# Kernel optimization log

Hardware: AMD Instinct MI355X
Metric: run time of the kernel (lower is better)

The kernel has to match this reference:

```python
import jax, jax.numpy as jnp
import numpy as np

B, CI, HW, K, C, NH, L = 512, 3, 28, 28 // 28 and 0 or 7, 1024, 16, 12
K = 7


def setup_inputs() -> dict:
    key = jax.random.key(0)
    ks = jax.random.split(key, 8)
    s = 0.02
    return {
        "x": jax.random.normal(ks[0], (B, CI, HW, HW), jnp.float32),
        "conv_w": jax.random.normal(ks[1], (C, CI, K, K), jnp.float32) * s,  # Conv2d weight [Co,Ci,k,k], shared with deconv
        "ln1_w": jnp.ones((L, C), jnp.float32),
        "ln1_b": jnp.zeros((L, C), jnp.float32),
        "wq": jax.random.normal(ks[2], (L, C, C), jnp.float32) * s,
        "wk": jax.random.normal(ks[3], (L, C, C), jnp.float32) * s,
        "wv": jax.random.normal(ks[4], (L, C, C), jnp.float32) * s,
        "ln2_w": jnp.ones((L, C), jnp.float32),
        "ln2_b": jnp.zeros((L, C), jnp.float32),
        "mlp_w": jax.random.normal(ks[5], (L, C, C), jnp.float32) * s,
        "mlp_b": jnp.zeros((L, C), jnp.float32),
        "out_w": jax.random.normal(ks[6], (C, C), jnp.float32) * s,
        "out_b": jnp.zeros((C,), jnp.float32),
        "head_num": NH,
    }


def _layernorm(x, w, b, eps=1e-5):
    m = jnp.mean(x, axis=-1, keepdims=True)
    v = jnp.var(x, axis=-1, keepdims=True)  # biased var, matches torch LayerNorm
    return (x - m) * jax.lax.rsqrt(v + eps) * w + b


def _attn(h, wq, wk, wv, nh):
    b, t, c = h.shape
    hd = c // nh
    q = (h @ wq.T).reshape(b, t, nh, hd).transpose(0, 2, 1, 3)  # [B,H,T,hd]
    k = (h @ wk.T).reshape(b, t, nh, hd).transpose(0, 2, 1, 3)
    v = (h @ wv.T).reshape(b, t, nh, hd).transpose(0, 2, 1, 3)
    scores = jnp.einsum("bhqd,bhkd->bhqk", q, k) / jnp.sqrt(jnp.float32(hd))
    mask = jnp.tril(jnp.ones((t, t), bool))
    scores = jnp.where(mask, scores, -jnp.inf)
    a = jax.nn.softmax(scores, axis=-1)
    o = jnp.einsum("bhqk,bhkd->bhqd", a, v)
    return o.transpose(0, 2, 1, 3).reshape(b, t, c)


def _forward(x, conv_w, ln1_w, ln1_b, wq, wk, wv, ln2_w, ln2_b, mlp_w, mlp_b, out_w, out_b, head_num):
    b, ci, hh, ww = x.shape
    co, _, k, _ = conv_w.shape
    # thumbnail: bilinear downsample to (k,k) (align_corners=False == half-pixel), then k-strided conv -> [B,Co]
    thumb = jax.image.resize(x, (b, ci, k, k), method="bilinear", antialias=False)
    thumb_tok = jnp.einsum("bcpq,dcpq->bd", thumb, conv_w)
    # kernel==stride conv == patchify + matmul
    hp, wp = hh // k, ww // k
    xp = x.reshape(b, ci, hp, k, wp, k)
    patches = jnp.einsum("bcipjq,dcpq->bdij", xp, conv_w).reshape(b, co, hp * wp)
    h = jnp.concatenate([thumb_tok[:, :, None], patches], axis=-1).transpose(0, 2, 1)  # [B,T=1+hp*wp,C]
    nlayers = ln1_w.shape[0]
    for l in range(nlayers):
        a = _attn(_layernorm(h, ln1_w[l], ln1_b[l]), wq[l], wk[l], wv[l], head_num)
        h = h + a
        m = _layernorm(h, ln2_w[l], ln2_b[l]) @ mlp_w[l].T + mlp_b[l]
        h = h + m
    logits = h @ out_w.T + out_b  # [B,T,C]
    # decode: ConvTranspose2d(kernel=stride=k) with shared weight; input [B,Co,1,T] -> [B,Ci,k,T*k]
    z = logits.transpose(0, 2, 1)  # [B,Co,T]
    t = z.shape[-1]
    out = jnp.einsum("bcs,cdhw->bdhsw", z, conv_w).reshape(b, ci, k, t * k)
    return out


def reference(x, conv_w, ln1_w, ln1_b, wq, wk, wv, ln2_w, ln2_b, mlp_w, mlp_b, out_w, out_b, head_num):
    return _forward(x, conv_w, ln1_w, ln1_b, wq, wk, wv, ln2_w, ln2_b, mlp_w, mlp_b, out_w, out_b, head_num)
```

## Files before the change

### kernel.cpp

```cpp
#include <hip/hip_runtime.h>


typedef unsigned short u16;
typedef short bfrag8 __attribute__((ext_vector_type(8)));
typedef float facc4 __attribute__((ext_vector_type(4)));

__device__ __forceinline__ u16 f2bf(float f) {
  union { float f; unsigned u; } x; x.f = f;
  unsigned r = x.u + 0x7fffu + ((x.u >> 16) & 1u);
  return (u16)(r >> 16);
}
__device__ __forceinline__ float bf2f(u16 h) {
  union { unsigned u; float f; } x; x.u = ((unsigned)h) << 16;
  return x.f;
}


template <int QM>
__device__ __forceinline__ void loadA(const u16* S, int sb, int aBase, int swz,
                                      bfrag8 (&aF)[4][2])
{
  const int base = sb + QM * 8192 + aBase;
#pragma unroll
  for (int im = 0; im < 4; ++im) {
    aF[im][0] = *(const bfrag8*)&S[base + im * 1024 + swz];
    aF[im][1] = *(const bfrag8*)&S[base + im * 1024 + (swz ^ 32)];
  }
}

template <int QN>
__device__ __forceinline__ void loadB(const u16* S, int sb, int bBase, int swz,
                                      bfrag8 (&bF)[2][2])
{
  const int base = sb + 16384 + QN * 8192 + bBase;
#pragma unroll
  for (int in = 0; in < 2; ++in) {
    bF[in][0] = *(const bfrag8*)&S[base + in * 1024 + swz];
    bF[in][1] = *(const bfrag8*)&S[base + in * 1024 + (swz ^ 32)];
  }
}

template <int QM, int QN>
__device__ __forceinline__ void pmfma(bfrag8 (&aF)[4][2], bfrag8 (&bF)[2][2],
                                      facc4 (&acc)[8][4])
{
#pragma unroll
  for (int im = 0; im < 4; ++im)
#pragma unroll
    for (int in = 0; in < 2; ++in) {
      facc4 c = acc[QM * 4 + im][QN * 2 + in];
      c = __builtin_amdgcn_mfma_f32_16x16x32_bf16(aF[im][0], bF[in][0], c, 0, 0, 0);
      c = __builtin_amdgcn_mfma_f32_16x16x32_bf16(aF[im][1], bF[in][1], c, 0, 0, 0);
      acc[QM * 4 + im][QN * 2 + in] = c;
    }
}

template <int MODE>
__global__ __launch_bounds__(512, 2) void gemm256(
    const u16* __restrict__ A, int lda,
    const u16* __restrict__ B0, const u16* __restrict__ B1, const u16* __restrict__ B2,
    int ldb, int K, int cpx,
    void* __restrict__ outp, long long zstride, int ldo,
    const float* __restrict__ bias)
{
  __shared__ u16 S[65536];

  const int bid = blockIdx.x;
  const int wg = (bid & 7) * cpx + (bid >> 3);
  const int perz = 34 * 4;
  const int z = wg / perz;
  const int r0 = wg - z * perz;
  const int y = r0 >> 2;
  const int x = r0 & 3;
  const int m0 = y * 256, n0 = x * 256;
  const u16* __restrict__ B = (z == 0) ? B0 : ((z == 1) ? B1 : B2);

  const int tid = threadIdx.x;
  const int wave = tid >> 6;
  const int lane = tid & 63;
  const int lrow = lane & 15, lquad = lane >> 4;
  const int mh = wave >> 2;
  const int w4 = wave & 3;
  const int wm = mh * 128, wn = w4 * 64;

  const int swz = (lquad ^ (lrow & 7)) * 8;
  const int aBase = mh * 4096 + lrow * 64;
  const int bBase = w4 * 2048 + lrow * 64;

  const int l3 = lane >> 3;
  const int kc = ((lane & 7) ^ l3) * 8;
  const int arow0 = mh * 128 + (wave & 3) * 16 + l3;
  const int arow1 = arow0 + 8;
  const int w20 = wave * 2, w21 = wave * 2 + 1;
  const int brow0 = (w20 >> 2) * 64 + (w20 & 3) * 8 + l3;
  const int brow1 = (w21 >> 2) * 64 + (w21 & 3) * 8 + l3;
  const u16* gA0 = A + (long long)(m0 + arow0) * lda + kc;
  const u16* gA1 = A + (long long)(m0 + arow1) * lda + kc;
  const u16* gB0 = B + (long long)(n0 + brow0) * ldb + kc;
  const u16* gB1 = B + (long long)(n0 + brow1) * ldb + kc;
  const long long aq = 64LL * lda;
  const long long bq = 32LL * ldb;
  const int ldsW = wave * 1024 + lane * 8;

  auto stageA = [&](int qm, int tt) {
    u16* d0 = S + ((tt & 1) * 32768 + qm * 8192) + ldsW;
    __builtin_amdgcn_global_load_lds((const __attribute__((address_space(1))) void*)(gA0 + qm * aq + tt * 64),
                                     (__attribute__((address_space(3))) void*)d0, 16, 0, 0);
    __builtin_amdgcn_global_load_lds((const __attribute__((address_space(1))) void*)(gA1 + qm * aq + tt * 64),
                                     (__attribute__((address_space(3))) void*)(d0 + 512), 16, 0, 0);
  };
  auto stageB = [&](int qn, int tt) {
    u16* d0 = S + ((tt & 1) * 32768 + 16384 + qn * 8192) + ldsW;
    __builtin_amdgcn_global_load_lds((const __attribute__((address_space(1))) void*)(gB0 + qn * bq + tt * 64),
                                     (__attribute__((address_space(3))) void*)d0, 16, 0, 0);
    __builtin_amdgcn_global_load_lds((const __attribute__((address_space(1))) void*)(gB1 + qn * bq + tt * 64),
                                     (__attribute__((address_space(3))) void*)(d0 + 512), 16, 0, 0);
  };

  facc4 acc[8][4] = {};

  stageA(0, 0); stageB(0, 0); stageA(1, 0); stageB(1, 0); stageA(0, 1);
  asm volatile("s_waitcnt vmcnt(6)" ::: "memory");
  __builtin_amdgcn_sched_barrier(0);
  __builtin_amdgcn_s_barrier();

  const int NT = K >> 6;
  bfrag8 aF[4][2], bF[2][2];
  for (int t = 0; t < NT; ++t) {
    const int sb = (t & 1) * 32768;
    {
      loadA<0>(S, sb, aBase, swz, aF);
      loadB<0>(S, sb, bBase, swz, bF);
      if (t + 1 < NT) stageB(0, t + 1);
      __builtin_amdgcn_sched_barrier(0);
      __builtin_amdgcn_s_barrier();
      asm volatile("s_waitcnt lgkmcnt(0)" ::: "memory");
      __builtin_amdgcn_sched_barrier(0);
      __builtin_amdgcn_s_setprio(1);
      pmfma<0, 0>(aF, bF, acc);
      __builtin_amdgcn_s_setprio(0);
      if (t + 1 < NT) asm volatile("s_waitcnt vmcnt(4)" ::: "memory");
      else            asm volatile("s_waitcnt vmcnt(0)" ::: "memory");
      __builtin_amdgcn_sched_barrier(0);
      __builtin_amdgcn_s_barrier();
    }
    {
      loadB<1>(S, sb, bBase, swz, bF);
      if (t + 1 < NT) stageA(1, t + 1);
      __builtin_amdgcn_sched_barrier(0);
      __builtin_amdgcn_s_barrier();
      asm volatile("s_waitcnt lgkmcnt(0)" ::: "memory");
      __builtin_amdgcn_sched_barrier(0);
      __builtin_amdgcn_s_setprio(1);
      pmfma<0, 1>(aF, bF, acc);
      __builtin_amdgcn_s_setprio(0);
      __builtin_amdgcn_sched_barrier(0);
      __builtin_amdgcn_s_barrier();
    }
    {
      loadA<1>(S, sb, aBase, swz, aF);
      if (t + 1 < NT) stageB(1, t + 1);
      __builtin_amdgcn_sched_barrier(0);
      __builtin_amdgcn_s_barrier();
      asm volatile("s_waitcnt lgkmcnt(0)" ::: "memory");
      __builtin_amdgcn_sched_barrier(0);
      __builtin_amdgcn_s_setprio(1);
      pmfma<1, 1>(aF, bF, acc);
      __builtin_amdgcn_s_setprio(0);
      if (t + 2 < NT) asm volatile("s_waitcnt vmcnt(4)" ::: "memory");
      else            asm volatile("s_waitcnt vmcnt(0)" ::: "memory");
      __builtin_amdgcn_sched_barrier(0);
      __builtin_amdgcn_s_barrier();
    }
    {
      loadB<0>(S, sb, bBase, swz, bF);
      if (t + 2 < NT) stageA(0, t + 2);
      __builtin_amdgcn_sched_barrier(0);
      __builtin_amdgcn_s_barrier();
      asm volatile("s_waitcnt lgkmcnt(0)" ::: "memory");
      __builtin_amdgcn_sched_barrier(0);
      __builtin_amdgcn_s_setprio(1);
      pmfma<1, 0>(aF, bF, acc);
      __builtin_amdgcn_s_setprio(0);
      __builtin_amdgcn_sched_barrier(0);
      __builtin_amdgcn_s_barrier();
    }
  }

#pragma unroll
  for (int in = 0; in < 4; ++in) {
    const int col = n0 + wn + in * 16 + lrow;
    const float bb = bias ? bias[col] : 0.0f;
#pragma unroll
    for (int im = 0; im < 8; ++im) {
#pragma unroll
      for (int r = 0; r < 4; ++r) {
        const int row = m0 + wm + im * 16 + lquad * 4 + r;
        const float v = acc[im][in][r] + bb;
        if (MODE == 1) {
          (((u16*)outp) + zstride * z)[(long long)row * ldo + col] = f2bf(v);
        } else if (MODE == 2) {
          ((float*)outp)[(long long)row * ldo + col] += v;
        } else {
          const long long off = (long long)row * ldo + col;
          const float nv = ((float*)outp)[off] + v;
          ((float*)outp)[off] = nv;
          ((u16*)zstride)[off] = f2bf(nv);
        }
      }
    }
  }
}

template <int MODE>
__global__ __launch_bounds__(256) void gemm_bt(
    const u16* __restrict__ A, int lda,
    const u16* __restrict__ B0, const u16* __restrict__ B1, const u16* __restrict__ B2,
    int ldb, int K, int NX,
    void* __restrict__ outp, long long zstride, int ldo,
    const float* __restrict__ bias)
{
  __shared__ __align__(16) u16 As[8192];
  __shared__ __align__(16) u16 Bs[8192];

  const int l = blockIdx.x;
  const int xcd = l & 7;
  const int j = l >> 3;
  const int per_epoch = 9 * NX;
  const int z = j / per_epoch;
  const int r2 = j - z * per_epoch;
  const int g = r2 / NX;
  const int y = xcd + 8 * g;
  if (y >= 68) return;
  const int x = r2 - g * NX;
  const int n0 = x * 128;
  const int m0 = y * 128;
  const u16* __restrict__ B = (z == 0) ? B0 : ((z == 1) ? B1 : B2);

  const int tid  = threadIdx.x;
  const int wave = tid >> 6;
  const int lane = tid & 63;
  const int wm   = (wave >> 1) * 64;
  const int wn   = (wave & 1) * 64;
  const int lrow = lane & 15;
  const int lquad = lane >> 4;

  facc4 acc[4][4] = {};

  const u16* ga[4]; const u16* gb[4];
#pragma unroll
  for (int j2 = 0; j2 < 4; ++j2) {
    const int s = tid + 256 * j2;
    const int t = s >> 9, s2 = s & 511;
    const int r = s2 >> 2, c = (s2 & 3) + 4 * t;
    ga[j2] = A + (long long)(m0 + r) * lda + c * 8;
    gb[j2] = B + (long long)(n0 + r) * ldb + c * 8;
  }

  const int aoff = (wm + lrow) * 32 + lquad * 8;
  const int boff = (wn + lrow) * 32 + lquad * 8;

  for (int k0 = 0; k0 < K; k0 += 64) {
#pragma unroll
    for (int j2 = 0; j2 < 4; ++j2) {
      __builtin_amdgcn_global_load_lds((const __attribute__((address_space(1))) void*)ga[j2],
                                       (__attribute__((address_space(3))) void*)(As + (tid + 256 * j2) * 8), 16, 0, 0);
      __builtin_amdgcn_global_load_lds((const __attribute__((address_space(1))) void*)gb[j2],
                                       (__attribute__((address_space(3))) void*)(Bs + (tid + 256 * j2) * 8), 16, 0, 0);
      ga[j2] += 64; gb[j2] += 64;
    }
    __syncthreads();

#pragma unroll
    for (int t = 0; t < 2; ++t) {
      bfrag8 af[4], bfr[4];
#pragma unroll
      for (int im = 0; im < 4; ++im) af[im] = *(const bfrag8*)(As + t * 4096 + aoff + 512 * im);
#pragma unroll
      for (int in = 0; in < 4; ++in) bfr[in] = *(const bfrag8*)(Bs + t * 4096 + boff + 512 * in);
#pragma unroll
      for (int im = 0; im < 4; ++im)
#pragma unroll
        for (int in = 0; in < 4; ++in)
          acc[im][in] = __builtin_amdgcn_mfma_f32_16x16x32_bf16(af[im], bfr[in], acc[im][in], 0, 0, 0);
    }
    __syncthreads();
  }

#pragma unroll
  for (int in = 0; in < 4; ++in) {
    const int col = n0 + wn + in * 16 + lrow;
    const float bb = bias ? bias[col] : 0.0f;
#pragma unroll
    for (int im = 0; im < 4; ++im) {
#pragma unroll
      for (int r = 0; r < 4; ++r) {
        const int row = m0 + wm + im * 16 + lquad * 4 + r;
        const float v = acc[im][in][r] + bb;
        if (MODE == 0) {
          ((float*)outp)[(long long)row * ldo + col] = v;
        } else if (MODE == 1) {
          (((u16*)outp) + zstride * z)[(long long)row * ldo + col] = f2bf(v);
        } else if (MODE == 2) {
          ((float*)outp)[(long long)row * ldo + col] += v;
        } else if (MODE == 4) {
          const long long off = (long long)row * ldo + col;
          const float nv = ((float*)outp)[off] + v;
          ((float*)outp)[off] = nv;
          ((u16*)zstride)[off] = f2bf(nv);
        } else {
          if (col < 147) {
            const int b = row / 17, s = row - b * 17;
            const int d = col / 49, rem = col - d * 49;
            const int hk = rem / 7, wk = rem - hk * 7;
            ((float*)outp)[(long long)((b * 3 + d) * 7 + hk) * 119 + s * 7 + wk] = v;
          }
        }
      }
    }
  }
}

__global__ __launch_bounds__(256) void ln_kernel(
    const float* __restrict__ h, const float* __restrict__ w,
    const float* __restrict__ b, u16* __restrict__ out)
{
  const long long row = blockIdx.x;
  const int t = threadIdx.x;
  const float4 v = ((const float4*)(h + row * 1024))[t];
  float s = v.x + v.y + v.z + v.w;
  float q = v.x * v.x + v.y * v.y + v.z * v.z + v.w * v.w;
  for (int o = 32; o > 0; o >>= 1) { s += __shfl_down(s, o); q += __shfl_down(q, o); }
  __shared__ float ss[4], sq[4];
  const int wave = t >> 6, lane = t & 63;
  if (lane == 0) { ss[wave] = s; sq[wave] = q; }
  __syncthreads();
  const float st = ss[0] + ss[1] + ss[2] + ss[3];
  const float qt = sq[0] + sq[1] + sq[2] + sq[3];
  const float mean = st * (1.0f / 1024.0f);
  const float var = qt * (1.0f / 1024.0f) - mean * mean;
  const float inv = rsqrtf(var + 1e-5f);
  const float4 w4 = ((const float4*)w)[t];
  const float4 b4 = ((const float4*)b)[t];
  ushort4 o;
  o.x = f2bf((v.x - mean) * inv * w4.x + b4.x);
  o.y = f2bf((v.y - mean) * inv * w4.y + b4.y);
  o.z = f2bf((v.z - mean) * inv * w4.z + b4.z);
  o.w = f2bf((v.w - mean) * inv * w4.w + b4.w);
  ((ushort4*)(out + row * 1024))[t] = o;
}

__global__ __launch_bounds__(256) void attn_kernel(const u16* __restrict__ QKV,
                                                   float* __restrict__ h)
{
  const int blk = blockIdx.x;
  const int b = blk >> 4, head = blk & 15;
  __shared__ float qs[17][64], ks[17][64], vs[17][64];
  __shared__ float sc[17][20];
  const long long base = (long long)b * 17408 + head * 64;
  const u16* Q  = QKV;
  const u16* Kp = QKV + 8912896LL;
  const u16* V  = QKV + 17825792LL;
  const int tid = threadIdx.x;

  if (tid < 136) {
    const int t = tid >> 3, dg = (tid & 7) * 8;
    const long long off = base + (long long)t * 1024 + dg;
    union { uint4 u; u16 s[8]; } xq, xk, xv;
    xq.u = *(const uint4*)(Q + off);
    xk.u = *(const uint4*)(Kp + off);
    xv.u = *(const uint4*)(V + off);
#pragma unroll
    for (int j = 0; j < 8; ++j) {
      qs[t][dg + j] = bf2f(xq.s[j]);
      ks[t][dg + j] = bf2f(xk.s[j]);
      vs[t][dg + j] = bf2f(xv.s[j]);
    }
  }
  __syncthreads();

  for (int i = tid; i < 289; i += 256) {
    const int tq = i / 17, tk = i % 17;
    float a = 0.0f;
    if (tk <= tq) {
#pragma unroll
      for (int d = 0; d < 64; ++d) a += qs[tq][d] * ks[tk][d];
      a *= 0.125f;
    }
    sc[tq][tk] = a;
  }
  __syncthreads();

  if (tid < 17) {
    const int tq = tid;
    float m = -1e30f;
    for (int tk = 0; tk <= tq; ++tk) m = fmaxf(m, sc[tq][tk]);
    float s = 0.0f;
    for (int tk = 0; tk <= tq; ++tk) { const float e = __expf(sc[tq][tk] - m); sc[tq][tk] = e; s += e; }
    const float inv = 1.0f / s;
    for (int tk = 0; tk <= tq; ++tk) sc[tq][tk] *= inv;
  }
  __syncthreads();

  for (int i = tid; i < 272; i += 256) {
    const int tq = i >> 4, dg = (i & 15) * 4;
    float o0 = 0, o1 = 0, o2 = 0, o3 = 0;
    for (int tk = 0; tk <= tq; ++tk) {
      const float s = sc[tq][tk];
      o0 += s * vs[tk][dg];     o1 += s * vs[tk][dg + 1];
      o2 += s * vs[tk][dg + 2]; o3 += s * vs[tk][dg + 3];
    }
    float4* hp = (float4*)(h + base + (long long)tq * 1024 + dg);
    float4 hv = *hp;
    hv.x += o0; hv.y += o1; hv.z += o2; hv.w += o3;
    *hp = hv;
  }
}

__global__ void build_p(const float* __restrict__ x, u16* __restrict__ P)
{
  const int n = blockIdx.x;
  const int j = threadIdx.x;
  if (j >= 192) return;
  const int b = n / 17, t = n % 17;
  float val = 0.0f;
  if (j < 147) {
    const int c = j / 49, rem = j % 49, p = rem / 7, q = rem % 7;
    const float* xb = x + (long long)(b * 3 + c) * 784;
    if (t == 0) {
      const int r = 4 * p + 1, cc = 4 * q + 1;
      val = 0.25f * (xb[r * 28 + cc] + xb[r * 28 + cc + 1] +
                     xb[(r + 1) * 28 + cc] + xb[(r + 1) * 28 + cc + 1]);
    } else {
      const int s = t - 1, ii = s >> 2, jj = s & 3;
      val = xb[(7 * ii + p) * 28 + 7 * jj + q];
    }
  }
  P[(long long)n * 192 + j] = f2bf(val);
}

__global__ __launch_bounds__(256) void cvt_conv(const float* __restrict__ cw,
                                                u16* __restrict__ Wc, u16* __restrict__ cw2)
{
  const int i = blockIdx.x * 256 + threadIdx.x;
  if (i < 196608) {
    const int d = i / 192, j = i % 192;
    Wc[i] = (j < 147) ? f2bf(cw[d * 147 + j]) : (u16)0;
  } else {
    const int i2 = i - 196608;
    if (i2 < 262144) {
      const int j = i2 / 1024, c = i2 % 1024;
      cw2[i2] = (j < 147) ? f2bf(cw[c * 147 + j]) : (u16)0;
    }
  }
}

__global__ __launch_bounds__(256) void wprime_kernel(
    const u16* __restrict__ cw2, const float* __restrict__ outw,
    u16* __restrict__ Wp)
{
  const int k = blockIdx.x * 256 + threadIdx.x;
  const int j = blockIdx.y;
  float a = 0.0f;
  for (int c = 0; c < 1024; ++c)
    a += bf2f(cw2[j * 1024 + c]) * outw[c * 1024 + k];
  Wp[j * 1024 + k] = f2bf(a);
}

__global__ __launch_bounds__(256) void bprime_kernel(
    const u16* __restrict__ cw2, const float* __restrict__ outb,
    float* __restrict__ bp)
{
  const int j = threadIdx.x;
  float a = 0.0f;
  for (int c = 0; c < 1024; ++c) a += outb[c] * bf2f(cw2[j * 1024 + c]);
  bp[j] = a;
}

__global__ __launch_bounds__(256) void cvt_all(
    const float* __restrict__ wq, const float* __restrict__ wk,
    const float* __restrict__ wv, const float* __restrict__ mlpw,
    const float* __restrict__ outw, u16* __restrict__ wAll)
{
  const int i = blockIdx.x * 256 + threadIdx.x;
  const int which = i >> 18;
  const int off = i & 262143;
  const float4* src;
  if (which < 48) {
    const int layer = which >> 2, sub = which & 3;
    const float* base = (sub == 0) ? wq : (sub == 1) ? wk : (sub == 2) ? wv : mlpw;
    src = (const float4*)(base + (size_t)layer * 1048576) + off;
  } else {
    src = (const float4*)outw + off;
  }
  const float4 v = *src;
  ushort4 o; o.x = f2bf(v.x); o.y = f2bf(v.y); o.z = f2bf(v.z); o.w = f2bf(v.w);
  *(ushort4*)(wAll + (size_t)which * 1048576 + (size_t)off * 4) = o;
}

__global__ __launch_bounds__(256) void cvt4(const float* __restrict__ a0, const float* __restrict__ a1,
                                            const float* __restrict__ a2, const float* __restrict__ a3,
                                            u16* __restrict__ o3, u16* __restrict__ om)
{
  const int i = blockIdx.x * 256 + threadIdx.x;
  const int which = i >> 20, off = i & 1048575;
  const float* src = (which == 0) ? a0 : (which == 1) ? a1 : (which == 2) ? a2 : a3;
  const float v = src[off];
  if (which < 3) o3[which * 1048576 + off] = f2bf(v);
  else           om[off] = f2bf(v);
}

__global__ __launch_bounds__(256) void cvtN(const float* __restrict__ in, u16* __restrict__ out, int n)
{
  const int i = blockIdx.x * 256 + threadIdx.x;
  if (i < n) out[i] = f2bf(in[i]);
}

extern "C" void kernel_launch(void* const* d_in, const int* in_sizes, int n_in,
                              void* d_out, int out_size, void* d_ws, size_t ws_size,
                              hipStream_t stream)
{
  const float* x     = (const float*)d_in[0];
  const float* convw = (const float*)d_in[1];
  const float* ln1w  = (const float*)d_in[2];
  const float* ln1b  = (const float*)d_in[3];
  const float* wq    = (const float*)d_in[4];
  const float* wk    = (const float*)d_in[5];
  const float* wv    = (const float*)d_in[6];
  const float* ln2w  = (const float*)d_in[7];
  const float* ln2b  = (const float*)d_in[8];
  const float* mlpw  = (const float*)d_in[9];
  const float* mlpb  = (const float*)d_in[10];
  const float* outw  = (const float*)d_in[11];
  const float* outb  = (const float*)d_in[12];

  char* w = (char*)d_ws;
  const bool big = (ws_size >= 214500352ULL);

  const int G_QKV = 8 * 3 * 9 * 8;
  const int G_ONE = 8 * 1 * 9 * 8;
  const int G_DEC = 8 * 1 * 9 * 2;

  if (big) {
    float* h   = (float*)(w);
    u16* Abuf  = (u16*)(w + 35651584);
    u16* QKV   = (u16*)(w + 53477376);
    u16* wAll  = (u16*)(w + 106954752);
    u16* Wc    = (u16*)(w + 209715200);
    u16* cw2   = (u16*)(w + 210108416);
    u16* P     = (u16*)(w + 210632704);
    u16* Wp    = (u16*)(w + 213975040);
    float* bp  = (float*)(w + 214499328);

    cvt_all<<<50176, 256, 0, stream>>>(wq, wk, wv, mlpw, outw, wAll);
    cvt_conv<<<1792, 256, 0, stream>>>(convw, Wc, cw2);
    wprime_kernel<<<dim3(4, 256), 256, 0, stream>>>(cw2, outw, Wp);
    bprime_kernel<<<1, 256, 0, stream>>>(cw2, outb, bp);
    build_p<<<8704, 192, 0, stream>>>(x, P);
    gemm_bt<0><<<G_ONE, 256, 0, stream>>>(P, 192, Wc, Wc, Wc, 192, 192, 8,
                                          (void*)h, 0LL, 1024, nullptr);
    for (int l = 0; l < 12; ++l) {
      u16* wl = wAll + (size_t)l * 4194304;
      ln_kernel<<<8704, 256, 0, stream>>>(h, ln1w + l * 1024, ln1b + l * 1024, Abuf);
      gemm256<1><<<408, 512, 0, stream>>>(Abuf, 1024, wl, wl + 1048576, wl + 2097152,
                                          1024, 1024, 51, (void*)QKV, 8912896LL, 1024, nullptr);
      attn_kernel<<<8192, 256, 0, stream>>>(QKV, h);
      ln_kernel<<<8704, 256, 0, stream>>>(h, ln2w + l * 1024, ln2b + l * 1024, Abuf);
      if (l < 11) {
        gemm_bt<2><<<G_ONE, 256, 0, stream>>>(Abuf, 1024, wl + 3145728, wl, wl,
                                              1024, 1024, 8, (void*)h, 0LL, 1024, mlpb + l * 1024);
      } else {
        gemm_bt<4><<<G_ONE, 256, 0, stream>>>(Abuf, 1024, wl + 3145728, wl, wl,
                                              1024, 1024, 8, (void*)h,
                                              (long long)(uintptr_t)QKV, 1024,
                                              mlpb + l * 1024);
      }
    }
    gemm_bt<3><<<G_DEC, 256, 0, stream>>>(QKV, 1024, Wp, Wp, Wp,
                                          1024, 1024, 2, d_out, 0LL, 0, bp);
  } else {
    if (ws_size < 119603200ULL) return;
    float* h   = (float*)(w);
    u16* Abuf  = (u16*)(w + 35651584);
    u16* QKV   = (u16*)(w + 53477376);
    u16* wb3   = (u16*)(w + 106954752);
    u16* wmb   = (u16*)(w + 113246208);
    u16* Wc    = (u16*)(w + 115343360);
    u16* cw2   = (u16*)(w + 115736576);
    u16* P     = (u16*)(w + 116260864);

    cvt_conv<<<1792, 256, 0, stream>>>(convw, Wc, cw2);
    build_p<<<8704, 192, 0, stream>>>(x, P);
    gemm_bt<0><<<G_ONE, 256, 0, stream>>>(P, 192, Wc, Wc, Wc, 192, 192, 8,
                                          (void*)h, 0LL, 1024, nullptr);
    for (int l = 0; l < 12; ++l) {
      const size_t wo = (size_t)l * 1048576;
      cvt4<<<16384, 256, 0, stream>>>(wq + wo, wk + wo, wv + wo, mlpw + wo, wb3, wmb);
      ln_kernel<<<8704, 256, 0, stream>>>(h, ln1w + l * 1024, ln1b + l * 1024, Abuf);
      gemm_bt<1><<<G_QKV, 256, 0, stream>>>(Abuf, 1024, wb3, wb3 + 1048576, wb3 + 2097152,
                                            1024, 1024, 8, (void*)QKV, 8912896LL, 1024, nullptr);
      attn_kernel<<<8192, 256, 0, stream>>>(QKV, h);
      ln_kernel<<<8704, 256, 0, stream>>>(h, ln2w + l * 1024, ln2b + l * 1024, Abuf);
      gemm_bt<2><<<G_ONE, 256, 0, stream>>>(Abuf, 1024, wmb, wmb, wmb,
                                            1024, 1024, 8, (void*)h, 0LL, 1024, mlpb + l * 1024);
    }
    cvtN<<<34816, 256, 0, stream>>>(h, Abuf, 8912896);
    cvtN<<<4096, 256, 0, stream>>>(outw, wmb, 1048576);
    gemm_bt<1><<<G_ONE, 256, 0, stream>>>(Abuf, 1024, wmb, wmb, wmb,
                                          1024, 1024, 8, (void*)QKV, 0LL, 1024, outb);
    gemm_bt<3><<<G_DEC, 256, 0, stream>>>(QKV, 1024, cw2, cw2, cw2,
                                          1024, 1024, 2, d_out, 0LL, 0, nullptr);
  }
}
```

Baseline: 2.771 ms.

## Restructure gemm256 pipeline with double B fragments and route MLP GEMM through it

Reorders the global-to-LDS staging in the 256-tile GEMM main loop so each stage waits on vmcnt before its barrier. It keeps two separate B fragment register sets so the fourth MFMA phase reuses already-loaded B data instead of reloading from LDS. This removes one LDS read pass and several barriers per K-step. The MLP GEMM (and the final fused MLP+out variant) now uses the larger gemm256 kernel with 136 blocks instead of gemm_bt, cutting tile reloads at the cost of fewer, larger workgroups and more registers.

```diff
diff --git a/kernel.cpp b/kernel.cpp
--- a/kernel.cpp
+++ b/kernel.cpp
@@ -119,71 +119,62 @@
 
   facc4 acc[8][4] = {};
 
-  stageA(0, 0); stageB(0, 0); stageA(1, 0); stageB(1, 0); stageA(0, 1);
-  asm volatile("s_waitcnt vmcnt(6)" ::: "memory");
+  stageA(0, 0); stageB(0, 0); stageB(1, 0); stageA(1, 0);
+  asm volatile("s_waitcnt vmcnt(4)" ::: "memory");
   __builtin_amdgcn_sched_barrier(0);
   __builtin_amdgcn_s_barrier();
 
   const int NT = K >> 6;
-  bfrag8 aF[4][2], bF[2][2];
+  bfrag8 aF[4][2], b0[2][2], b1[2][2];
   for (int t = 0; t < NT; ++t) {
     const int sb = (t & 1) * 32768;
+    const bool more = (t + 1 < NT);
     {
       loadA<0>(S, sb, aBase, swz, aF);
-      loadB<0>(S, sb, bBase, swz, bF);
-      if (t + 1 < NT) stageB(0, t + 1);
+      loadB<0>(S, sb, bBase, swz, b0);
+      if (more) stageA(0, t + 1);
+      if (more) asm volatile("s_waitcnt vmcnt(4)" ::: "memory");
+      else      asm volatile("s_waitcnt vmcnt(2)" ::: "memory");
       __builtin_amdgcn_sched_barrier(0);
       __builtin_amdgcn_s_barrier();
       asm volatile("s_waitcnt lgkmcnt(0)" ::: "memory");
       __builtin_amdgcn_sched_barrier(0);
       __builtin_amdgcn_s_setprio(1);
-      pmfma<0, 0>(aF, bF, acc);
+      pmfma<0, 0>(aF, b0, acc);
       __builtin_amdgcn_s_setprio(0);
-      if (t + 1 < NT) asm volatile("s_waitcnt vmcnt(4)" ::: "memory");
-      else            asm volatile("s_waitcnt vmcnt(0)" ::: "memory");
-      __builtin_amdgcn_sched_barrier(0);
-      __builtin_amdgcn_s_barrier();
     }
     {
-      loadB<1>(S, sb, bBase, swz, bF);
-      if (t + 1 < NT) stageA(1, t + 1);
+      loadB<1>(S, sb, bBase, swz, b1);
+      if (more) stageB(0, t + 1);
+      if (more) asm volatile("s_waitcnt vmcnt(4)" ::: "memory");
+      else      asm volatile("s_waitcnt vmcnt(0)" ::: "memory");
       __builtin_amdgcn_sched_barrier(0);
       __builtin_amdgcn_s_barrier();
       asm volatile("s_waitcnt lgkmcnt(0)" ::: "memory");
       __builtin_amdgcn_sched_barrier(0);
       __builtin_amdgcn_s_setprio(1);
-      pmfma<0, 1>(aF, bF, acc);
+      pmfma<0, 1>(aF, b1, acc);
       __builtin_amdgcn_s_setprio(0);
-      __builtin_amdgcn_sched_barrier(0);
-      __builtin_amdgcn_s_barrier();
     }
     {
       loadA<1>(S, sb, aBase, swz, aF);
-      if (t + 1 < NT) stageB(1, t + 1);
+      if (more) stageB(1, t + 1);
       __builtin_amdgcn_sched_barrier(0);
       __builtin_amdgcn_s_barrier();
       asm volatile("s_waitcnt lgkmcnt(0)" ::: "memory");
       __builtin_amdgcn_sched_barrier(0);
       __builtin_amdgcn_s_setprio(1);
-      pmfma<1, 1>(aF, bF, acc);
+      pmfma<1, 1>(aF, b1, acc);
       __builtin_amdgcn_s_setprio(0);
-      if (t + 2 < NT) asm volatile("s_waitcnt vmcnt(4)" ::: "memory");
-      else            asm volatile("s_waitcnt vmcnt(0)" ::: "memory");
+    }
+    {
+      if (more) stageA(1, t + 1);
+      if (more) asm volatile("s_waitcnt vmcnt(4)" ::: "memory");
       __builtin_amdgcn_sched_barrier(0);
       __builtin_amdgcn_s_barrier();
-    }
-    {
-      loadB<0>(S, sb, bBase, swz, bF);
-      if (t + 2 < NT) stageA(0, t + 2);
-      __builtin_amdgcn_sched_barrier(0);
-      __builtin_amdgcn_s_barrier();
-      asm volatile("s_waitcnt lgkmcnt(0)" ::: "memory");
-      __builtin_amdgcn_sched_barrier(0);
       __builtin_amdgcn_s_setprio(1);
-      pmfma<1, 0>(aF, bF, acc);
+      pmfma<1, 0>(aF, b0, acc);
       __builtin_amdgcn_s_setprio(0);
-      __builtin_amdgcn_sched_barrier(0);
-      __builtin_amdgcn_s_barrier();
     }
   }
 
@@ -567,13 +558,13 @@
       attn_kernel<<<8192, 256, 0, stream>>>(QKV, h);
       ln_kernel<<<8704, 256, 0, stream>>>(h, ln2w + l * 1024, ln2b + l * 1024, Abuf);
       if (l < 11) {
-        gemm_bt<2><<<G_ONE, 256, 0, stream>>>(Abuf, 1024, wl + 3145728, wl, wl,
-                                              1024, 1024, 8, (void*)h, 0LL, 1024, mlpb + l * 1024);
+        gemm256<2><<<136, 512, 0, stream>>>(Abuf, 1024, wl + 3145728, wl + 3145728, wl + 3145728,
+                                            1024, 1024, 17, (void*)h, 0LL, 1024, mlpb + l * 1024);
       } else {
-        gemm_bt<4><<<G_ONE, 256, 0, stream>>>(Abuf, 1024, wl + 3145728, wl, wl,
-                                              1024, 1024, 8, (void*)h,
-                                              (long long)(uintptr_t)QKV, 1024,
-                                              mlpb + l * 1024);
+        gemm256<4><<<136, 512, 0, stream>>>(Abuf, 1024, wl + 3145728, wl + 3145728, wl + 3145728,
+                                            1024, 1024, 17, (void*)h,
+                                            (long long)(uintptr_t)QKV, 1024,
+                                            mlpb + l * 1024);
       }
     }
     gemm_bt<3><<<G_DEC, 256, 0, stream>>>(QKV, 1024, Wp, Wp, Wp,
```

Result: no change. 2.777 ms (+0.2%).
